# Kernel optimization log

Measured on AMD Instinct MI355X. Metric: run time of the kernel, lower is better.

Reference implementation:

```python
import jax, jax.numpy as jnp
import numpy as np

N_NODES = 10000
N_EDGES = 80000
LATENT = 128
OUT_SIZE = 3
NODE_F = 12
EDGE_F = 7
STEPS = 15
LN_EPS = 1e-5


def _mlp(x, W0, b0, W1, b1, W2, b2):
    h = jax.nn.relu(x @ W0 + b0)
    h = jax.nn.relu(h @ W1 + b1)
    return h @ W2 + b2


def _ln(x, g, b):
    m = jnp.mean(x, axis=-1, keepdims=True)
    v = jnp.mean(jnp.square(x - m), axis=-1, keepdims=True)
    return (x - m) * jax.lax.rsqrt(v + LN_EPS) * g + b


def _forward(node_features, edge_features, senders, receivers,
             enW0, enb0, enW1, enb1, enW2, enb2, eng, enbe,
             eeW0, eeb0, eeW1, eeb1, eeW2, eeb2, eeg, eebe,
             beW0, beb0, beW1, beb1, beW2, beb2, beg, bebe,
             bnW0, bnb0, bnW1, bnb1, bnW2, bnb2, bng, bnbe,
             dW0, db0, dW1, db1, dW2, db2):
    # Encoder: node and mesh-edge MLPs with LayerNorm
    nl = _ln(_mlp(node_features, enW0, enb0, enW1, enb1, enW2, enb2), eng, enbe)  # [N, L]
    el = _ln(_mlp(edge_features, eeW0, eeb0, eeW1, eeb1, eeW2, eeb2), eeg, eebe)  # [E, L]

    # Processor: 15 GraphNetBlocks with residual connections, scanned over stacked params
    def block(carry, p):
        n, e = carry
        (eW0, eb0, eW1, eb1, eW2, eb2, eg, ebe,
         nW0, nb0, nW1, nb1, nW2, nb2, ng, nbe) = p
        feat = jnp.concatenate([n[senders], n[receivers], e], axis=-1)  # [E, 3L]
        new_e = _ln(_mlp(feat, eW0, eb0, eW1, eb1, eW2, eb2), eg, ebe)  # [E, L]
        agg = jax.ops.segment_sum(new_e, receivers, num_segments=N_NODES)  # [N, L]
        new_n = _ln(_mlp(jnp.concatenate([n, agg], axis=-1), nW0, nb0, nW1, nb1, nW2, nb2), ng, nbe)
        return (n + new_n, e + new_e), None

    xs = (beW0, beb0, beW1, beb1, beW2, beb2, beg, bebe,
          bnW0, bnb0, bnW1, bnb1, bnW2, bnb2, bng, bnbe)
    (nl, el), _ = jax.lax.scan(jax.checkpoint(block), (nl, el), xs)

    # Decoder: MLP without LayerNorm
    return _mlp(nl, dW0, db0, dW1, db1, dW2, db2)  # [N, OUT_SIZE]


def setup_inputs() -> dict:
    ks = iter(jax.random.split(jax.random.key(0), 32))

    def W(*shape):
        return jax.random.normal(next(ks), shape, jnp.float32) * (1.0 / np.sqrt(shape[-2]))

    z = lambda *s: jnp.zeros(s, jnp.float32)
    o = lambda *s: jnp.ones(s, jnp.float32)
    d = {}
    d['node_features'] = jax.random.normal(next(ks), (N_NODES, NODE_F), jnp.float32)
    d['edge_features'] = jax.random.normal(next(ks), (N_EDGES, EDGE_F), jnp.float32)
    d['senders'] = jax.random.randint(next(ks), (N_EDGES,), 0, N_NODES, jnp.int32)
    d['receivers'] = jax.random.randint(next(ks), (N_EDGES,), 0, N_NODES, jnp.int32)
    d.update(enW0=W(NODE_F, LATENT), enb0=z(LATENT), enW1=W(LATENT, LATENT), enb1=z(LATENT),
             enW2=W(LATENT, LATENT), enb2=z(LATENT), eng=o(LATENT), enbe=z(LATENT))
    d.update(eeW0=W(EDGE_F, LATENT), eeb0=z(LATENT), eeW1=W(LATENT, LATENT), eeb1=z(LATENT),
             eeW2=W(LATENT, LATENT), eeb2=z(LATENT), eeg=o(LATENT), eebe=z(LATENT))
    d.update(beW0=W(STEPS, 3 * LATENT, LATENT), beb0=z(STEPS, LATENT),
             beW1=W(STEPS, LATENT, LATENT), beb1=z(STEPS, LATENT),
             beW2=W(STEPS, LATENT, LATENT), beb2=z(STEPS, LATENT),
             beg=o(STEPS, LATENT), bebe=z(STEPS, LATENT))
    d.update(bnW0=W(STEPS, 2 * LATENT, LATENT), bnb0=z(STEPS, LATENT),
             bnW1=W(STEPS, LATENT, LATENT), bnb1=z(STEPS, LATENT),
             bnW2=W(STEPS, LATENT, LATENT), bnb2=z(STEPS, LATENT),
             bng=o(STEPS, LATENT), bnbe=z(STEPS, LATENT))
    d.update(dW0=W(LATENT, LATENT), db0=z(LATENT), dW1=W(LATENT, LATENT), db1=z(LATENT),
             dW2=W(LATENT, OUT_SIZE), db2=z(OUT_SIZE))
    return d


def reference(node_features, edge_features, senders, receivers,
              enW0, enb0, enW1, enb1, enW2, enb2, eng, enbe,
              eeW0, eeb0, eeW1, eeb1, eeW2, eeb2, eeg, eebe,
              beW0, beb0, beW1, beb1, beW2, beb2, beg, bebe,
              bnW0, bnb0, bnW1, bnb1, bnW2, bnb2, bng, bnbe,
              dW0, db0, dW1, db1, dW2, db2):
    return _forward(node_features, edge_features, senders, receivers,
                    enW0, enb0, enW1, enb1, enW2, enb2, eng, enbe,
                    eeW0, eeb0, eeW1, eeb1, eeW2, eeb2, eeg, eebe,
                    beW0, beb0, beW1, beb1, beW2, beb2, beg, bebe,
                    bnW0, bnb0, bnW1, bnb1, bnW2, bnb2, bng, bnbe,
                    dW0, db0, dW1, db1, dW2, db2)
```

## Files before the change

### kernel.cpp

```cpp
#include <hip/hip_runtime.h>
#include <hip/hip_bf16.h>
#include <stdint.h>

#define N_NODES 10000
#define N_EDGES 80000
#define L 128
#define STEPS 15
#define LN_EPS 1e-5f
#define NTHR 256
#define BM 128

#define H_STRIDE 272
#define H_WAVE   8704
#define WS_OFF   34816
#define LDS_SZ   45056

typedef short short8 __attribute__((ext_vector_type(8)));
typedef float floatx4 __attribute__((ext_vector_type(4)));

__device__ __forceinline__ float bf2f(const __hip_bfloat16 x) {
    return __bfloat162float(x);
}
__device__ __forceinline__ float ldmix(const void* p, int idx, int isf32) {
    return isf32 ? ((const float*)p)[idx]
                 : bf2f(((const __hip_bfloat16*)p)[idx]);
}

__global__ void detect_dtype(const uint32_t* __restrict__ nf, int* cnt) {
    int c = 0;
    for (int i = blockIdx.x * blockDim.x + threadIdx.x; i < 60000;
         i += gridDim.x * blockDim.x) {
        const uint32_t w = nf[i];
        c += (((w >> 7) & 0xFF) >= 0xC6) + (((w >> 23) & 0xFF) >= 0xC6);
    }
    atomicAdd(cnt, c);
}

#define N_TMATS 14
struct TAll {
    const void* src[N_TMATS];
    long long cum[N_TMATS + 1];
    int K[N_TMATS], N[N_TMATS], Kpad[N_TMATS];
};

__global__ void transpose_all(TAll a, const int* __restrict__ cnt,
                              __hip_bfloat16* __restrict__ pool) {
    const int isf32 = (*cnt > 1000);
    const long long total = a.cum[N_TMATS];
    for (long long i = blockIdx.x * (long long)blockDim.x + threadIdx.x;
         i < total; i += gridDim.x * (long long)blockDim.x) {
        int e = 0;
        #pragma unroll 1
        for (int j = 1; j < N_TMATS; j++) if (i >= a.cum[j]) e = j;
        const long long r = i - a.cum[e];
        const int per = a.N[e] * a.Kpad[e];
        const int m = (int)(r / per);
        const int r2 = (int)(r - (long long)m * per);
        const int nn = r2 / a.Kpad[e];
        const int kk = r2 - nn * a.Kpad[e];
        float v = 0.f;
        if (kk < a.K[e]) v = ldmix(a.src[e], (m * a.K[e] + kk) * a.N[e] + nn, isf32);
        pool[i] = __float2bfloat16(v);
    }
}

__global__ void convert_feats(const void* __restrict__ nf,
                              const void* __restrict__ ef,
                              const int* __restrict__ cnt,
                              __hip_bfloat16* __restrict__ fN,
                              __hip_bfloat16* __restrict__ fE)
{
    const int isf32 = (*cnt > 1000);
    const int totN = N_NODES * 32;
    const int totE = N_EDGES * 32;
    for (int i = blockIdx.x * blockDim.x + threadIdx.x; i < totN + totE;
         i += gridDim.x * blockDim.x) {
        if (i < totN) {
            const int r = i >> 5, c = i & 31;
            fN[i] = __float2bfloat16(c < 12 ? ldmix(nf, r * 12 + c, isf32) : 0.f);
        } else {
            const int j = i - totN;
            const int r = j >> 5, c = j & 31;
            fE[j] = __float2bfloat16(c < 7 ? ldmix(ef, r * 7 + c, isf32) : 0.f);
        }
    }
}

__global__ void csr_hist(const int* __restrict__ rcv, int* __restrict__ deg) {
    for (int i = blockIdx.x * blockDim.x + threadIdx.x; i < N_EDGES;
         i += gridDim.x * blockDim.x)
        atomicAdd(&deg[rcv[i]], 1);
}

__global__ void csr_scan(const int* __restrict__ deg, int* __restrict__ rowptr,
                         int* __restrict__ cursor) {
    __shared__ int part[256];
    __shared__ int partx[257];
    const int t = threadIdx.x;
    int s = 0;
    for (int j = 0; j < 40; j++) {
        const int i = t * 40 + j;
        if (i < N_NODES) s += deg[i];
    }
    part[t] = s;
    __syncthreads();
    if (t == 0) {
        int r = 0;
        for (int k = 0; k < 256; k++) { partx[k] = r; r += part[k]; }
        partx[256] = r;
    }
    __syncthreads();
    int run = partx[t];
    for (int j = 0; j < 40; j++) {
        const int i = t * 40 + j;
        if (i < N_NODES) {
            rowptr[i] = run;
            cursor[i] = run;
            run += deg[i];
        }
    }
    if (t == 255) rowptr[N_NODES] = partx[256];
}

__global__ void csr_scatter(const int* __restrict__ rcv, int* __restrict__ cursor,
                            int* __restrict__ elist) {
    for (int i = blockIdx.x * blockDim.x + threadIdx.x; i < N_EDGES;
         i += gridDim.x * blockDim.x) {
        const int p = atomicAdd(&cursor[rcv[i]], 1);
        elist[p] = i;
    }
}

__global__ __launch_bounds__(256)
void csr_agg(const int* __restrict__ rowptr, const int* __restrict__ elist,
             const __hip_bfloat16* __restrict__ ln16,
             __hip_bfloat16* __restrict__ agg16)
{
    const int g = threadIdx.x >> 5;
    const int lane = threadIdx.x & 31;
    const int v = blockIdx.x * 8 + g;
    if (v >= N_NODES) return;
    const int c0 = lane * 4;
    float s0 = 0.f, s1 = 0.f, s2 = 0.f, s3 = 0.f;
    const int b = rowptr[v], en = rowptr[v + 1];
    for (int j = b; j < en; j++) {
        const int e = elist[j];
        union { uint2 w; __hip_bfloat16 h[4]; } u;
        u.w = *(const uint2*)(ln16 + (size_t)e * L + c0);
        s0 += bf2f(u.h[0]); s1 += bf2f(u.h[1]);
        s2 += bf2f(u.h[2]); s3 += bf2f(u.h[3]);
    }
    union { uint2 w; __hip_bfloat16 h[4]; } o;
    o.h[0] = __float2bfloat16(s0); o.h[1] = __float2bfloat16(s1);
    o.h[2] = __float2bfloat16(s2); o.h[3] = __float2bfloat16(s3);
    *(uint2*)(agg16 + (size_t)v * L + c0) = o.w;
}

enum AMode { A_PLAIN = 0, A_FEAT = 1, A_CAT = 2 };
enum Epi   { E_LN_STORE = 0, E_LN_EDGE = 1, E_LN_NODE = 2, E_DEC = 3 };

template <int AMODE, int EPI, int NL>
__global__ __launch_bounds__(NTHR, 2)
void fused_mlp(const __hip_bfloat16* __restrict__ A, int lda, int M, int K0,
               const __hip_bfloat16* __restrict__ WT0,
               const __hip_bfloat16* __restrict__ WT1,
               const __hip_bfloat16* __restrict__ WT2,
               const void* __restrict__ b0,
               const void* __restrict__ b1,
               const void* __restrict__ b2,
               const void* __restrict__ g,
               const void* __restrict__ beta,
               int poff,
               const int* __restrict__ cnt,
               const __hip_bfloat16* __restrict__ n16,
               const __hip_bfloat16* __restrict__ e16s,
               const __hip_bfloat16* __restrict__ agg16,
               const int* __restrict__ snd,
               const int* __restrict__ rcv,
               float* __restrict__ res32,
               __hip_bfloat16* __restrict__ res16,
               __hip_bfloat16* __restrict__ ln16,
               const void* __restrict__ dW,
               const void* __restrict__ db,
               void* __restrict__ dout)
{
    __shared__ __align__(16) char lds[LDS_SZ];
    char* AsB = lds;
    char* WsB = lds + WS_OFF;

    const int tid  = threadIdx.x;
    const int wv   = tid >> 6;
    const int lane = tid & 63;
    const int quad = lane >> 4;
    const int m15  = lane & 15;
    const int row0 = blockIdx.x * BM;
    const int isf32 = (*cnt > 1000);

    char* hw = lds + wv * H_WAVE;

    const int aoff0 = (wv * 32 + m15) * 80 + quad * 16;
    const int aoff1 = aoff0 + 16 * 80;
    const int boff  = m15 * 80 + quad * 16;

    floatx4 acc[2][8];

    #pragma unroll
    for (int rt = 0; rt < 2; rt++)
        #pragma unroll
        for (int ct = 0; ct < 8; ct++) acc[rt][ct] = (floatx4)0.f;

    for (int k0 = 0; k0 < K0; k0 += 32) {
        #pragma unroll
        for (int i2 = 0; i2 < 2; i2++) {
            const int flat = i2 * NTHR + tid;
            const int ar = flat >> 2;
            const int aq = flat & 3;
            const int rg = row0 + ar;
            int4 av = make_int4(0, 0, 0, 0);
            if (rg < M) {
                if constexpr (AMODE == A_PLAIN) {
                    av = *(const int4*)(A + (size_t)rg * lda + k0 + aq * 8);
                } else if constexpr (AMODE == A_FEAT) {
                    const __hip_bfloat16* sp;
                    if (k0 < L)          sp = n16  + (size_t)snd[rg] * L + k0 + aq * 8;
                    else if (k0 < 2 * L) sp = n16  + (size_t)rcv[rg] * L + (k0 - L) + aq * 8;
                    else                 sp = e16s + (size_t)rg * L + (k0 - 2 * L) + aq * 8;
                    av = *(const int4*)sp;
                } else {
                    const __hip_bfloat16* sp = (k0 < L)
                        ? n16   + (size_t)rg * L + k0 + aq * 8
                        : agg16 + (size_t)rg * L + (k0 - L) + aq * 8;
                    av = *(const int4*)sp;
                }
            }
            *(int4*)(AsB + ar * 80 + aq * 16) = av;
            *(int4*)(WsB + ar * 80 + aq * 16) =
                *(const int4*)(WT0 + (size_t)ar * K0 + k0 + aq * 8);
        }
        __syncthreads();
        const short8 a0 = *(const short8*)(AsB + aoff0);
        const short8 a1 = *(const short8*)(AsB + aoff1);
        #pragma unroll
        for (int ct = 0; ct < 8; ct++) {
            const short8 b = *(const short8*)(WsB + boff + ct * 1280);
            acc[0][ct] = __builtin_amdgcn_mfma_f32_16x16x32_bf16(a0, b, acc[0][ct], 0, 0, 0);
            acc[1][ct] = __builtin_amdgcn_mfma_f32_16x16x32_bf16(a1, b, acc[1][ct], 0, 0, 0);
        }
        __syncthreads();
    }
    {
        float bb[8];
        #pragma unroll
        for (int ct = 0; ct < 8; ct++) bb[ct] = ldmix(b0, poff + ct * 16 + m15, isf32);
        #pragma unroll
        for (int rt = 0; rt < 2; rt++)
            #pragma unroll
            for (int ct = 0; ct < 8; ct++)
                #pragma unroll
                for (int i = 0; i < 4; i++) {
                    const int rl = rt * 16 + quad * 4 + i;
                    const int col = ct * 16 + m15;
                    *(__hip_bfloat16*)(hw + rl * H_STRIDE + col * 2) =
                        __float2bfloat16(fmaxf(acc[rt][ct][i] + bb[ct], 0.f));
                }
    }

    {
        #pragma unroll
        for (int rt = 0; rt < 2; rt++)
            #pragma unroll
            for (int ct = 0; ct < 8; ct++) acc[rt][ct] = (floatx4)0.f;
        short8 af[2][4];
        #pragma unroll
        for (int rt = 0; rt < 2; rt++)
            #pragma unroll
            for (int c = 0; c < 4; c++)
                af[rt][c] = *(const short8*)(hw + (rt * 16 + m15) * H_STRIDE + c * 64 + quad * 16);
        for (int c = 0; c < 4; c++) {
            #pragma unroll
            for (int i2 = 0; i2 < 2; i2++) {
                const int flat = i2 * NTHR + tid;
                const int ar = flat >> 2;
                const int aq = flat & 3;
                *(int4*)(WsB + ar * 80 + aq * 16) =
                    *(const int4*)(WT1 + (size_t)ar * L + c * 32 + aq * 8);
            }
            __syncthreads();
            #pragma unroll
            for (int ct = 0; ct < 8; ct++) {
                const short8 b = *(const short8*)(WsB + boff + ct * 1280);
                acc[0][ct] = __builtin_amdgcn_mfma_f32_16x16x32_bf16(af[0][c], b, acc[0][ct], 0, 0, 0);
                acc[1][ct] = __builtin_amdgcn_mfma_f32_16x16x32_bf16(af[1][c], b, acc[1][ct], 0, 0, 0);
            }
            __syncthreads();
        }
        float bb[8];
        #pragma unroll
        for (int ct = 0; ct < 8; ct++) bb[ct] = ldmix(b1, poff + ct * 16 + m15, isf32);
        #pragma unroll
        for (int rt = 0; rt < 2; rt++)
            #pragma unroll
            for (int ct = 0; ct < 8; ct++)
                #pragma unroll
                for (int i = 0; i < 4; i++) {
                    const int rl = rt * 16 + quad * 4 + i;
                    const int col = ct * 16 + m15;
                    *(__hip_bfloat16*)(hw + rl * H_STRIDE + col * 2) =
                        __float2bfloat16(fmaxf(acc[rt][ct][i] + bb[ct], 0.f));
                }
    }

    if constexpr (NL == 3) {
        #pragma unroll
        for (int rt = 0; rt < 2; rt++)
            #pragma unroll
            for (int ct = 0; ct < 8; ct++) acc[rt][ct] = (floatx4)0.f;
        short8 af[2][4];
        #pragma unroll
        for (int rt = 0; rt < 2; rt++)
            #pragma unroll
            for (int c = 0; c < 4; c++)
                af[rt][c] = *(const short8*)(hw + (rt * 16 + m15) * H_STRIDE + c * 64 + quad * 16);
        for (int c = 0; c < 4; c++) {
            #pragma unroll
            for (int i2 = 0; i2 < 2; i2++) {
                const int flat = i2 * NTHR + tid;
                const int ar = flat >> 2;
                const int aq = flat & 3;
                *(int4*)(WsB + ar * 80 + aq * 16) =
                    *(const int4*)(WT2 + (size_t)ar * L + c * 32 + aq * 8);
            }
            __syncthreads();
            #pragma unroll
            for (int ct = 0; ct < 8; ct++) {
                const short8 b = *(const short8*)(WsB + boff + ct * 1280);
                acc[0][ct] = __builtin_amdgcn_mfma_f32_16x16x32_bf16(af[0][c], b, acc[0][ct], 0, 0, 0);
                acc[1][ct] = __builtin_amdgcn_mfma_f32_16x16x32_bf16(af[1][c], b, acc[1][ct], 0, 0, 0);
            }
            __syncthreads();
        }
        float bb[8], gg[8], be[8];
        #pragma unroll
        for (int ct = 0; ct < 8; ct++) {
            bb[ct] = ldmix(b2,   poff + ct * 16 + m15, isf32);
            gg[ct] = ldmix(g,    poff + ct * 16 + m15, isf32);
            be[ct] = ldmix(beta, poff + ct * 16 + m15, isf32);
        }
        #pragma unroll
        for (int rt = 0; rt < 2; rt++) {
            #pragma unroll
            for (int i = 0; i < 4; i++) {
                float t[8], s = 0.f, s2 = 0.f;
                #pragma unroll
                for (int ct = 0; ct < 8; ct++) {
                    t[ct] = acc[rt][ct][i] + bb[ct];
                    s  += t[ct];
                    s2 += t[ct] * t[ct];
                }
                #pragma unroll
                for (int m = 1; m < 16; m <<= 1) {
                    s  += __shfl_xor(s,  m, 64);
                    s2 += __shfl_xor(s2, m, 64);
                }
                const float mean = s * (1.f / 128.f);
                const float var  = s2 * (1.f / 128.f) - mean * mean;
                const float inv  = rsqrtf(fmaxf(var, 0.f) + LN_EPS);
                const int rl = wv * 32 + rt * 16 + quad * 4 + i;
                const int rg = row0 + rl;
                if (rg < M) {
                    #pragma unroll
                    for (int ct = 0; ct < 8; ct++) {
                        const int col = ct * 16 + m15;
                        const float o = (t[ct] - mean) * inv * gg[ct] + be[ct];
                        const size_t idx = (size_t)rg * L + col;
                        if constexpr (EPI == E_LN_STORE) {
                            res32[idx] = o;
                            res16[idx] = __float2bfloat16(o);
                        } else if constexpr (EPI == E_LN_NODE) {
                            const float nw = res32[idx] + o;
                            res32[idx] = nw;
                            res16[idx] = __float2bfloat16(nw);
                        } else {
                            const float nw = res32[idx] + o;
                            res32[idx] = nw;
                            res16[idx] = __float2bfloat16(nw);
                            ln16[idx]  = __float2bfloat16(o);
                        }
                    }
                }
            }
        }
    } else {
        __syncthreads();
        float* Wl = (float*)WsB;
        for (int i = tid; i < 3 * L; i += NTHR) {
            const int o = i / L, k = i - o * L;
            Wl[o * L + k] = ldmix(dW, k * 3 + o, isf32);
        }
        __syncthreads();
        if (tid < BM) {
            const int rg = row0 + tid;
            if (rg < M) {
                const __hip_bfloat16* hr =
                    (const __hip_bfloat16*)(lds + (tid >> 5) * H_WAVE + (tid & 31) * H_STRIDE);
                float s0 = ldmix(db, 0, isf32);
                float s1 = ldmix(db, 1, isf32);
                float s2 = ldmix(db, 2, isf32);
                #pragma unroll 8
                for (int k = 0; k < L; k++) {
                    const float hv = bf2f(hr[k]);
                    s0 += hv * Wl[k];
                    s1 += hv * Wl[L + k];
                    s2 += hv * Wl[2 * L + k];
                }
                if (isf32) {
                    float* o = (float*)dout;
                    o[rg * 3 + 0] = s0; o[rg * 3 + 1] = s1; o[rg * 3 + 2] = s2;
                } else {
                    __hip_bfloat16* o = (__hip_bfloat16*)dout;
                    o[rg * 3 + 0] = __float2bfloat16(s0);
                    o[rg * 3 + 1] = __float2bfloat16(s1);
                    o[rg * 3 + 2] = __float2bfloat16(s2);
                }
            }
        }
    }
}

extern "C" void kernel_launch(void* const* d_in, const int* in_sizes, int n_in,
                              void* d_out, int out_size, void* d_ws, size_t ws_size,
                              hipStream_t stream)
{
    (void)in_sizes; (void)n_in; (void)out_size; (void)ws_size;
    const int* snd = (const int*)d_in[2];
    const int* rcv = (const int*)d_in[3];

    char* ws = (char*)d_ws;
    int* cnt = (int*)ws;                              ws += 256;
    auto takeB = [&](size_t el) {
        __hip_bfloat16* p = (__hip_bfloat16*)ws;
        ws += ((el * 2 + 255) & ~255ull);
        return p;
    };
    auto takeF = [&](size_t el) {
        float* p = (float*)ws;
        ws += ((el * 4 + 255) & ~255ull);
        return p;
    };
    auto takeI = [&](size_t el) {
        int* p = (int*)ws;
        ws += ((el * 4 + 255) & ~255ull);
        return p;
    };

    const int srcIdx[N_TMATS] = {4, 6, 8, 12, 14, 16, 20, 22, 24, 28, 30, 32, 36, 38};
    const int tK[N_TMATS]    = {12, 128, 128, 7, 128, 128, 384, 128, 128, 256, 128, 128, 128, 128};
    const int tKp[N_TMATS]   = {32, 128, 128, 32, 128, 128, 384, 128, 128, 256, 128, 128, 128, 128};
    const int tNm[N_TMATS]   = {1, 1, 1, 1, 1, 1, STEPS, STEPS, STEPS, STEPS, STEPS, STEPS, 1, 1};
    TAll ta;
    long long cum = 0;
    __hip_bfloat16* wmat[N_TMATS];
    __hip_bfloat16* wpool = (__hip_bfloat16*)ws;
    for (int j = 0; j < N_TMATS; j++) {
        ta.src[j] = d_in[srcIdx[j]];
        ta.cum[j] = cum;
        ta.K[j] = tK[j]; ta.N[j] = 128; ta.Kpad[j] = tKp[j];
        wmat[j] = wpool + cum;
        cum += (long long)tNm[j] * 128 * tKp[j];
    }
    ta.cum[N_TMATS] = cum;
    ws += ((cum * 2 + 255) & ~255ull);

    float* n32 = takeF((size_t)N_NODES * L);
    float* e32 = takeF((size_t)N_EDGES * L);
    __hip_bfloat16* n16   = takeB((size_t)N_NODES * L);
    __hip_bfloat16* e16   = takeB((size_t)N_EDGES * L);
    __hip_bfloat16* ln16  = takeB((size_t)N_EDGES * L);
    __hip_bfloat16* agg16 = takeB((size_t)N_NODES * L);
    __hip_bfloat16* fN16  = takeB((size_t)N_NODES * 32);
    __hip_bfloat16* fE16  = takeB((size_t)N_EDGES * 32);
    int* deg    = takeI(N_NODES);
    int* rowptr = takeI(N_NODES + 1);
    int* cursor = takeI(N_NODES);
    int* elist  = takeI(N_EDGES);

    const dim3 blk(NTHR);
    const dim3 grdE((N_EDGES + BM - 1) / BM);
    const dim3 grdN((N_NODES + BM - 1) / BM);

    (void)hipMemsetAsync(cnt, 0, sizeof(int), stream);
    (void)hipMemsetAsync(deg, 0, N_NODES * sizeof(int), stream);
    detect_dtype<<<dim3(64), blk, 0, stream>>>((const uint32_t*)d_in[0], cnt);
    convert_feats<<<dim3(256), blk, 0, stream>>>(d_in[0], d_in[1], cnt, fN16, fE16);
    transpose_all<<<dim3(512), blk, 0, stream>>>(ta, cnt, wpool);

    csr_hist<<<dim3(80), blk, 0, stream>>>(rcv, deg);
    csr_scan<<<dim3(1), blk, 0, stream>>>(deg, rowptr, cursor);
    csr_scatter<<<dim3(80), blk, 0, stream>>>(rcv, cursor, elist);

    fused_mlp<A_PLAIN, E_LN_STORE, 3><<<grdE, blk, 0, stream>>>(
        fE16, 32, N_EDGES, 32, wmat[3], wmat[4], wmat[5],
        d_in[13], d_in[15], d_in[17], d_in[18], d_in[19], 0, cnt,
        nullptr, nullptr, nullptr, nullptr, nullptr,
        e32, e16, nullptr, nullptr, nullptr, nullptr);
    fused_mlp<A_PLAIN, E_LN_STORE, 3><<<grdN, blk, 0, stream>>>(
        fN16, 32, N_NODES, 32, wmat[0], wmat[1], wmat[2],
        d_in[5], d_in[7], d_in[9], d_in[10], d_in[11], 0, cnt,
        nullptr, nullptr, nullptr, nullptr, nullptr,
        n32, n16, nullptr, nullptr, nullptr, nullptr);

    for (int s = 0; s < STEPS; s++) {
        const int po = s * L;
        fused_mlp<A_FEAT, E_LN_EDGE, 3><<<grdE, blk, 0, stream>>>(
            nullptr, 0, N_EDGES, 384,
            wmat[6] + (size_t)s * 128 * 384,
            wmat[7] + (size_t)s * 128 * 128,
            wmat[8] + (size_t)s * 128 * 128,
            d_in[21], d_in[23], d_in[25], d_in[26], d_in[27], po, cnt,
            n16, e16, nullptr, snd, rcv,
            e32, e16, ln16, nullptr, nullptr, nullptr);
        csr_agg<<<dim3((N_NODES + 7) / 8), blk, 0, stream>>>(rowptr, elist, ln16, agg16);
        fused_mlp<A_CAT, E_LN_NODE, 3><<<grdN, blk, 0, stream>>>(
            nullptr, 0, N_NODES, 256,
            wmat[9]  + (size_t)s * 128 * 256,
            wmat[10] + (size_t)s * 128 * 128,
            wmat[11] + (size_t)s * 128 * 128,
            d_in[29], d_in[31], d_in[33], d_in[34], d_in[35], po, cnt,
            n16, nullptr, agg16, nullptr, nullptr,
            n32, n16, nullptr, nullptr, nullptr, nullptr);
    }

    fused_mlp<A_PLAIN, E_DEC, 2><<<grdN, blk, 0, stream>>>(
        n16, L, N_NODES, L, wmat[12], wmat[13], nullptr,
        d_in[37], d_in[39], nullptr, nullptr, nullptr, 0, cnt,
        nullptr, nullptr, nullptr, nullptr, nullptr,
        nullptr, nullptr, nullptr, d_in[40], d_in[41], d_out);
}
```

Before: 1.433 ms.

## Fuse CSR aggregation into node MLP, prefetch tiles, drop bf16 edge copy

Removes the separate csr_agg kernel and computes each node tile's receiver-sum into LDS inside the node MLP kernel. The edge-latent bf16 copy is dropped: the edge MLP now reads the fp32 residual and converts it to bf16 on the fly. Global loads for A and W tiles are register-prefetched one k-step ahead, with gather indices hoisted. Node kernels use 64-row tiles via a new RT template parameter to raise block count. This saves launches and a bf16 edge write per step, at the cost of more LDS use and a doubled fp32 read in the edge kernel.

```diff
diff --git a/kernel.cpp b/kernel.cpp
--- a/kernel.cpp
+++ b/kernel.cpp
@@ -8,12 +8,7 @@
 #define STEPS 15
 #define LN_EPS 1e-5f
 #define NTHR 256
-#define BM 128
-
 #define H_STRIDE 272
-#define H_WAVE   8704
-#define WS_OFF   34816
-#define LDS_SZ   45056
 
 typedef short short8 __attribute__((ext_vector_type(8)));
 typedef float floatx4 __attribute__((ext_vector_type(4)));
@@ -131,35 +126,10 @@
     }
 }
 
-__global__ __launch_bounds__(256)
-void csr_agg(const int* __restrict__ rowptr, const int* __restrict__ elist,
-             const __hip_bfloat16* __restrict__ ln16,
-             __hip_bfloat16* __restrict__ agg16)
-{
-    const int g = threadIdx.x >> 5;
-    const int lane = threadIdx.x & 31;
-    const int v = blockIdx.x * 8 + g;
-    if (v >= N_NODES) return;
-    const int c0 = lane * 4;
-    float s0 = 0.f, s1 = 0.f, s2 = 0.f, s3 = 0.f;
-    const int b = rowptr[v], en = rowptr[v + 1];
-    for (int j = b; j < en; j++) {
-        const int e = elist[j];
-        union { uint2 w; __hip_bfloat16 h[4]; } u;
-        u.w = *(const uint2*)(ln16 + (size_t)e * L + c0);
-        s0 += bf2f(u.h[0]); s1 += bf2f(u.h[1]);
-        s2 += bf2f(u.h[2]); s3 += bf2f(u.h[3]);
-    }
-    union { uint2 w; __hip_bfloat16 h[4]; } o;
-    o.h[0] = __float2bfloat16(s0); o.h[1] = __float2bfloat16(s1);
-    o.h[2] = __float2bfloat16(s2); o.h[3] = __float2bfloat16(s3);
-    *(uint2*)(agg16 + (size_t)v * L + c0) = o.w;
-}
-
 enum AMode { A_PLAIN = 0, A_FEAT = 1, A_CAT = 2 };
 enum Epi   { E_LN_STORE = 0, E_LN_EDGE = 1, E_LN_NODE = 2, E_DEC = 3 };
 
-template <int AMODE, int EPI, int NL>
+template <int AMODE, int EPI, int NL, int RT>
 __global__ __launch_bounds__(NTHR, 2)
 void fused_mlp(const __hip_bfloat16* __restrict__ A, int lda, int M, int K0,
                const __hip_bfloat16* __restrict__ WT0,
@@ -172,79 +142,163 @@
                const void* __restrict__ beta,
                int poff,
                const int* __restrict__ cnt,
-               const __hip_bfloat16* __restrict__ n16,
-               const __hip_bfloat16* __restrict__ e16s,
-               const __hip_bfloat16* __restrict__ agg16,
+               const __hip_bfloat16* n16,
+               const __hip_bfloat16* lnsrc,
                const int* __restrict__ snd,
                const int* __restrict__ rcv,
-               float* __restrict__ res32,
-               __hip_bfloat16* __restrict__ res16,
-               __hip_bfloat16* __restrict__ ln16,
+               const int* __restrict__ rowptr,
+               const int* __restrict__ elist,
+               float* res32,
+               __hip_bfloat16* res16,
+               __hip_bfloat16* __restrict__ lnout,
                const void* __restrict__ dW,
                const void* __restrict__ db,
                void* __restrict__ dout)
 {
-    __shared__ __align__(16) char lds[LDS_SZ];
+    constexpr int BMv   = 64 * RT;
+    constexpr int HW    = RT * 16 * H_STRIDE;
+    constexpr int WSOFF = 4 * HW;
+    constexpr int LDSB  = WSOFF + 10240 + ((AMODE == A_CAT) ? BMv * 256 : 0);
+    __shared__ __align__(16) char lds[LDSB];
     char* AsB = lds;
-    char* WsB = lds + WS_OFF;
+    char* WsB = lds + WSOFF;
+    char* AgL = lds + WSOFF + 10240;
 
     const int tid  = threadIdx.x;
     const int wv   = tid >> 6;
     const int lane = tid & 63;
     const int quad = lane >> 4;
     const int m15  = lane & 15;
-    const int row0 = blockIdx.x * BM;
+    const int row0 = blockIdx.x * BMv;
     const int isf32 = (*cnt > 1000);
 
-    char* hw = lds + wv * H_WAVE;
-
-    const int aoff0 = (wv * 32 + m15) * 80 + quad * 16;
-    const int aoff1 = aoff0 + 16 * 80;
-    const int boff  = m15 * 80 + quad * 16;
-
-    floatx4 acc[2][8];
-
+    char* hw = lds + wv * HW;
+
+    const int boff = m15 * 80 + quad * 16;
+    int aoff[RT];
     #pragma unroll
-    for (int rt = 0; rt < 2; rt++)
+    for (int rt = 0; rt < RT; rt++)
+        aoff[rt] = (wv * 16 * RT + rt * 16 + m15) * 80 + quad * 16;
+
+    if constexpr (AMODE == A_CAT) {
+        const int half = tid >> 5, hl = tid & 31;
+        for (int v = half; v < BMv; v += 8) {
+            const int rg = row0 + v;
+            float s0 = 0.f, s1 = 0.f, s2 = 0.f, s3 = 0.f;
+            if (rg < M) {
+                int j = rowptr[rg];
+                const int en = rowptr[rg + 1];
+                for (; j + 3 < en; j += 4) {
+                    const int e0 = elist[j], e1 = elist[j+1], e2 = elist[j+2], e3 = elist[j+3];
+                    union { uint2 w; __hip_bfloat16 h[4]; } u0, u1, u2, u3;
+                    u0.w = *(const uint2*)(lnsrc + (size_t)e0 * L + hl * 4);
+                    u1.w = *(const uint2*)(lnsrc + (size_t)e1 * L + hl * 4);
+                    u2.w = *(const uint2*)(lnsrc + (size_t)e2 * L + hl * 4);
+                    u3.w = *(const uint2*)(lnsrc + (size_t)e3 * L + hl * 4);
+                    s0 += bf2f(u0.h[0]); s1 += bf2f(u0.h[1]); s2 += bf2f(u0.h[2]); s3 += bf2f(u0.h[3]);
+                    s0 += bf2f(u1.h[0]); s1 += bf2f(u1.h[1]); s2 += bf2f(u1.h[2]); s3 += bf2f(u1.h[3]);
+                    s0 += bf2f(u2.h[0]); s1 += bf2f(u2.h[1]); s2 += bf2f(u2.h[2]); s3 += bf2f(u2.h[3]);
+                    s0 += bf2f(u3.h[0]); s1 += bf2f(u3.h[1]); s2 += bf2f(u3.h[2]); s3 += bf2f(u3.h[3]);
+                }
+                for (; j < en; j++) {
+                    const int e = elist[j];
+                    union { uint2 w; __hip_bfloat16 h[4]; } u;
+                    u.w = *(const uint2*)(lnsrc + (size_t)e * L + hl * 4);
+                    s0 += bf2f(u.h[0]); s1 += bf2f(u.h[1]); s2 += bf2f(u.h[2]); s3 += bf2f(u.h[3]);
+                }
+            }
+            union { uint2 w; __hip_bfloat16 h[4]; } o;
+            o.h[0] = __float2bfloat16(s0); o.h[1] = __float2bfloat16(s1);
+            o.h[2] = __float2bfloat16(s2); o.h[3] = __float2bfloat16(s3);
+            *(uint2*)(AgL + v * 256 + hl * 8) = o.w;
+        }
+        __syncthreads();
+    }
+
+    const int aq = tid & 3;
+    int arow[RT], sidx[RT], ridx[RT];
+    #pragma unroll
+    for (int i2 = 0; i2 < RT; i2++) {
+        arow[i2] = (i2 * NTHR + tid) >> 2;
+        if constexpr (AMODE == A_FEAT) {
+            const int rg = row0 + arow[i2];
+            sidx[i2] = (rg < M) ? snd[rg] : 0;
+            ridx[i2] = (rg < M) ? rcv[rg] : 0;
+        }
+    }
+
+    auto loadA = [&](int k0, int i2) -> int4 {
+        const int ar = arow[i2];
+        const int rg = row0 + ar;
+        int4 av = make_int4(0, 0, 0, 0);
+        if (rg < M) {
+            if constexpr (AMODE == A_PLAIN) {
+                av = *(const int4*)(A + (size_t)rg * lda + k0 + aq * 8);
+            } else if constexpr (AMODE == A_FEAT) {
+                if (k0 < 2 * L) {
+                    const int nd = (k0 < L) ? sidx[i2] : ridx[i2];
+                    av = *(const int4*)(n16 + (size_t)nd * L + (k0 & (L - 1)) + aq * 8);
+                } else {
+                    const float* sp = res32 + (size_t)rg * L + (k0 - 2 * L) + aq * 8;
+                    const float4 f0 = *(const float4*)sp;
+                    const float4 f1 = *(const float4*)(sp + 4);
+                    union { int4 v; __hip_bfloat16 h[8]; } u;
+                    u.h[0] = __float2bfloat16(f0.x); u.h[1] = __float2bfloat16(f0.y);
+                    u.h[2] = __float2bfloat16(f0.z); u.h[3] = __float2bfloat16(f0.w);
+                    u.h[4] = __float2bfloat16(f1.x); u.h[5] = __float2bfloat16(f1.y);
+                    u.h[6] = __float2bfloat16(f1.z); u.h[7] = __float2bfloat16(f1.w);
+                    av = u.v;
+                }
+            } else {
+                if (k0 < L) av = *(const int4*)(n16 + (size_t)rg * L + k0 + aq * 8);
+                else        av = *(const int4*)(AgL + ar * 256 + (k0 - L) * 2 + aq * 16);
+            }
+        }
+        return av;
+    };
+    auto loadW = [&](const __hip_bfloat16* WT, int ksz, int k0, int i2) -> int4 {
+        const int flat = i2 * NTHR + tid;
+        return *(const int4*)(WT + (size_t)(flat >> 2) * ksz + k0 + (flat & 3) * 8);
+    };
+
+    floatx4 acc[RT][8];
+
+    #pragma unroll
+    for (int rt = 0; rt < RT; rt++)
         #pragma unroll
         for (int ct = 0; ct < 8; ct++) acc[rt][ct] = (floatx4)0.f;
 
+    int4 pA[RT], pW[2];
+    #pragma unroll
+    for (int i2 = 0; i2 < RT; i2++) pA[i2] = loadA(0, i2);
+    pW[0] = loadW(WT0, K0, 0, 0);
+    pW[1] = loadW(WT0, K0, 0, 1);
+
     for (int k0 = 0; k0 < K0; k0 += 32) {
+        #pragma unroll
+        for (int i2 = 0; i2 < RT; i2++)
+            *(int4*)(AsB + arow[i2] * 80 + aq * 16) = pA[i2];
         #pragma unroll
         for (int i2 = 0; i2 < 2; i2++) {
             const int flat = i2 * NTHR + tid;
-            const int ar = flat >> 2;
-            const int aq = flat & 3;
-            const int rg = row0 + ar;
-            int4 av = make_int4(0, 0, 0, 0);
-            if (rg < M) {
-                if constexpr (AMODE == A_PLAIN) {
-                    av = *(const int4*)(A + (size_t)rg * lda + k0 + aq * 8);
-                } else if constexpr (AMODE == A_FEAT) {
-                    const __hip_bfloat16* sp;
-                    if (k0 < L)          sp = n16  + (size_t)snd[rg] * L + k0 + aq * 8;
-                    else if (k0 < 2 * L) sp = n16  + (size_t)rcv[rg] * L + (k0 - L) + aq * 8;
-                    else                 sp = e16s + (size_t)rg * L + (k0 - 2 * L) + aq * 8;
-                    av = *(const int4*)sp;
-                } else {
-                    const __hip_bfloat16* sp = (k0 < L)
-                        ? n16   + (size_t)rg * L + k0 + aq * 8
-                        : agg16 + (size_t)rg * L + (k0 - L) + aq * 8;
-                    av = *(const int4*)sp;
-                }
-            }
-            *(int4*)(AsB + ar * 80 + aq * 16) = av;
-            *(int4*)(WsB + ar * 80 + aq * 16) =
-                *(const int4*)(WT0 + (size_t)ar * K0 + k0 + aq * 8);
+            *(int4*)(WsB + (flat >> 2) * 80 + (flat & 3) * 16) = pW[i2];
         }
         __syncthreads();
-        const short8 a0 = *(const short8*)(AsB + aoff0);
-        const short8 a1 = *(const short8*)(AsB + aoff1);
+        if (k0 + 32 < K0) {
+            #pragma unroll
+            for (int i2 = 0; i2 < RT; i2++) pA[i2] = loadA(k0 + 32, i2);
+            pW[0] = loadW(WT0, K0, k0 + 32, 0);
+            pW[1] = loadW(WT0, K0, k0 + 32, 1);
+        }
+        short8 a[RT];
+        #pragma unroll
+        for (int rt = 0; rt < RT; rt++) a[rt] = *(const short8*)(AsB + aoff[rt]);
         #pragma unroll
         for (int ct = 0; ct < 8; ct++) {
             const short8 b = *(const short8*)(WsB + boff + ct * 1280);
-            acc[0][ct] = __builtin_amdgcn_mfma_f32_16x16x32_bf16(a0, b, acc[0][ct], 0, 0, 0);
-            acc[1][ct] = __builtin_amdgcn_mfma_f32_16x16x32_bf16(a1, b, acc[1][ct], 0, 0, 0);
+            #pragma unroll
+            for (int rt = 0; rt < RT; rt++)
+                acc[rt][ct] = __builtin_amdgcn_mfma_f32_16x16x32_bf16(a[rt], b, acc[rt][ct], 0, 0, 0);
         }
         __syncthreads();
     }
@@ -253,7 +307,7 @@
         #pragma unroll
         for (int ct = 0; ct < 8; ct++) bb[ct] = ldmix(b0, poff + ct * 16 + m15, isf32);
         #pragma unroll
-        for (int rt = 0; rt < 2; rt++)
+        for (int rt = 0; rt < RT; rt++)
             #pragma unroll
             for (int ct = 0; ct < 8; ct++)
                 #pragma unroll
@@ -267,30 +321,35 @@
 
     {
         #pragma unroll
-        for (int rt = 0; rt < 2; rt++)
+        for (int rt = 0; rt < RT; rt++)
             #pragma unroll
             for (int ct = 0; ct < 8; ct++) acc[rt][ct] = (floatx4)0.f;
-        short8 af[2][4];
-        #pragma unroll
-        for (int rt = 0; rt < 2; rt++)
+        short8 af[RT][4];
+        #pragma unroll
+        for (int rt = 0; rt < RT; rt++)
             #pragma unroll
             for (int c = 0; c < 4; c++)
                 af[rt][c] = *(const short8*)(hw + (rt * 16 + m15) * H_STRIDE + c * 64 + quad * 16);
+        int4 qW[2];
+        qW[0] = loadW(WT1, L, 0, 0);
+        qW[1] = loadW(WT1, L, 0, 1);
         for (int c = 0; c < 4; c++) {
             #pragma unroll
             for (int i2 = 0; i2 < 2; i2++) {
                 const int flat = i2 * NTHR + tid;
-                const int ar = flat >> 2;
-                const int aq = flat & 3;
-                *(int4*)(WsB + ar * 80 + aq * 16) =
-                    *(const int4*)(WT1 + (size_t)ar * L + c * 32 + aq * 8);
+                *(int4*)(WsB + (flat >> 2) * 80 + (flat & 3) * 16) = qW[i2];
             }
             __syncthreads();
+            if (c < 3) {
+                qW[0] = loadW(WT1, L, (c + 1) * 32, 0);
+                qW[1] = loadW(WT1, L, (c + 1) * 32, 1);
+            }
             #pragma unroll
             for (int ct = 0; ct < 8; ct++) {
                 const short8 b = *(const short8*)(WsB + boff + ct * 1280);
-                acc[0][ct] = __builtin_amdgcn_mfma_f32_16x16x32_bf16(af[0][c], b, acc[0][ct], 0, 0, 0);
-                acc[1][ct] = __builtin_amdgcn_mfma_f32_16x16x32_bf16(af[1][c], b, acc[1][ct], 0, 0, 0);
+                #pragma unroll
+                for (int rt = 0; rt < RT; rt++)
+                    acc[rt][ct] = __builtin_amdgcn_mfma_f32_16x16x32_bf16(af[rt][c], b, acc[rt][ct], 0, 0, 0);
             }
             __syncthreads();
         }
@@ -298,7 +357,7 @@
         #pragma unroll
         for (int ct = 0; ct < 8; ct++) bb[ct] = ldmix(b1, poff + ct * 16 + m15, isf32);
         #pragma unroll
-        for (int rt = 0; rt < 2; rt++)
+        for (int rt = 0; rt < RT; rt++)
             #pragma unroll
             for (int ct = 0; ct < 8; ct++)
                 #pragma unroll
@@ -312,30 +371,35 @@
 
     if constexpr (NL == 3) {
         #pragma unroll
-        for (int rt = 0; rt < 2; rt++)
+        for (int rt = 0; rt < RT; rt++)
             #pragma unroll
             for (int ct = 0; ct < 8; ct++) acc[rt][ct] = (floatx4)0.f;
-        short8 af[2][4];
-        #pragma unroll
-        for (int rt = 0; rt < 2; rt++)
+        short8 af[RT][4];
+        #pragma unroll
+        for (int rt = 0; rt < RT; rt++)
             #pragma unroll
             for (int c = 0; c < 4; c++)
                 af[rt][c] = *(const short8*)(hw + (rt * 16 + m15) * H_STRIDE + c * 64 + quad * 16);
+        int4 qW[2];
+        qW[0] = loadW(WT2, L, 0, 0);
+        qW[1] = loadW(WT2, L, 0, 1);
         for (int c = 0; c < 4; c++) {
             #pragma unroll
             for (int i2 = 0; i2 < 2; i2++) {
                 const int flat = i2 * NTHR + tid;
-                const int ar = flat >> 2;
-                const int aq = flat & 3;
-                *(int4*)(WsB + ar * 80 + aq * 16) =
-                    *(const int4*)(WT2 + (size_t)ar * L + c * 32 + aq * 8);
+                *(int4*)(WsB + (flat >> 2) * 80 + (flat & 3) * 16) = qW[i2];
             }
             __syncthreads();
+            if (c < 3) {
+                qW[0] = loadW(WT2, L, (c + 1) * 32, 0);
+                qW[1] = loadW(WT2, L, (c + 1) * 32, 1);
+            }
             #pragma unroll
             for (int ct = 0; ct < 8; ct++) {
                 const short8 b = *(const short8*)(WsB + boff + ct * 1280);
-                acc[0][ct] = __builtin_amdgcn_mfma_f32_16x16x32_bf16(af[0][c], b, acc[0][ct], 0, 0, 0);
-                acc[1][ct] = __builtin_amdgcn_mfma_f32_16x16x32_bf16(af[1][c], b, acc[1][ct], 0, 0, 0);
+                #pragma unroll
+                for (int rt = 0; rt < RT; rt++)
+                    acc[rt][ct] = __builtin_amdgcn_mfma_f32_16x16x32_bf16(af[rt][c], b, acc[rt][ct], 0, 0, 0);
             }
             __syncthreads();
         }
@@ -347,7 +411,7 @@
             be[ct] = ldmix(beta, poff + ct * 16 + m15, isf32);
         }
         #pragma unroll
-        for (int rt = 0; rt < 2; rt++) {
+        for (int rt = 0; rt < RT; rt++) {
             #pragma unroll
             for (int i = 0; i < 4; i++) {
                 float t[8], s = 0.f, s2 = 0.f;
@@ -365,7 +429,7 @@
                 const float mean = s * (1.f / 128.f);
                 const float var  = s2 * (1.f / 128.f) - mean * mean;
                 const float inv  = rsqrtf(fmaxf(var, 0.f) + LN_EPS);
-                const int rl = wv * 32 + rt * 16 + quad * 4 + i;
+                const int rl = wv * 16 * RT + rt * 16 + quad * 4 + i;
                 const int rg = row0 + rl;
                 if (rg < M) {
                     #pragma unroll
@@ -375,7 +439,7 @@
                         const size_t idx = (size_t)rg * L + col;
                         if constexpr (EPI == E_LN_STORE) {
                             res32[idx] = o;
-                            res16[idx] = __float2bfloat16(o);
+                            if (res16) res16[idx] = __float2bfloat16(o);
                         } else if constexpr (EPI == E_LN_NODE) {
                             const float nw = res32[idx] + o;
                             res32[idx] = nw;
@@ -383,8 +447,7 @@
                         } else {
                             const float nw = res32[idx] + o;
                             res32[idx] = nw;
-                            res16[idx] = __float2bfloat16(nw);
-                            ln16[idx]  = __float2bfloat16(o);
+                            lnout[idx] = __float2bfloat16(o);
                         }
                     }
                 }
@@ -398,11 +461,13 @@
             Wl[o * L + k] = ldmix(dW, k * 3 + o, isf32);
         }
         __syncthreads();
-        if (tid < BM) {
+        if (tid < BMv) {
             const int rg = row0 + tid;
             if (rg < M) {
+                const int wave = tid / (16 * RT);
+                const int rw   = tid - wave * 16 * RT;
                 const __hip_bfloat16* hr =
-                    (const __hip_bfloat16*)(lds + (tid >> 5) * H_WAVE + (tid & 31) * H_STRIDE);
+                    (const __hip_bfloat16*)(lds + wave * HW + rw * H_STRIDE);
                 float s0 = ldmix(db, 0, isf32);
                 float s1 = ldmix(db, 1, isf32);
                 float s2 = ldmix(db, 2, isf32);
@@ -473,20 +538,18 @@
 
     float* n32 = takeF((size_t)N_NODES * L);
     float* e32 = takeF((size_t)N_EDGES * L);
-    __hip_bfloat16* n16   = takeB((size_t)N_NODES * L);
-    __hip_bfloat16* e16   = takeB((size_t)N_EDGES * L);
-    __hip_bfloat16* ln16  = takeB((size_t)N_EDGES * L);
-    __hip_bfloat16* agg16 = takeB((size_t)N_NODES * L);
-    __hip_bfloat16* fN16  = takeB((size_t)N_NODES * 32);
-    __hip_bfloat16* fE16  = takeB((size_t)N_EDGES * 32);
+    __hip_bfloat16* n16  = takeB((size_t)N_NODES * L);
+    __hip_bfloat16* ln16 = takeB((size_t)N_EDGES * L);
+    __hip_bfloat16* fN16 = takeB((size_t)N_NODES * 32);
+    __hip_bfloat16* fE16 = takeB((size_t)N_EDGES * 32);
     int* deg    = takeI(N_NODES);
     int* rowptr = takeI(N_NODES + 1);
     int* cursor = takeI(N_NODES);
     int* elist  = takeI(N_EDGES);
 
     const dim3 blk(NTHR);
-    const dim3 grdE((N_EDGES + BM - 1) / BM);
-    const dim3 grdN((N_NODES + BM - 1) / BM);
+    const dim3 grdE((N_EDGES + 127) / 128);
+    const dim3 grdN((N_NODES + 63) / 64);
 
     (void)hipMemsetAsync(cnt, 0, sizeof(int), stream);
     (void)hipMemsetAsync(deg, 0, N_NODES * sizeof(int), stream);
@@ -498,41 +561,40 @@
     csr_scan<<<dim3(1), blk, 0, stream>>>(deg, rowptr, cursor);
     csr_scatter<<<dim3(80), blk, 0, stream>>>(rcv, cursor, elist);
 
-    fused_mlp<A_PLAIN, E_LN_STORE, 3><<<grdE, blk, 0, stream>>>(
+    fused_mlp<A_PLAIN, E_LN_STORE, 3, 2><<<grdE, blk, 0, stream>>>(
         fE16, 32, N_EDGES, 32, wmat[3], wmat[4], wmat[5],
         d_in[13], d_in[15], d_in[17], d_in[18], d_in[19], 0, cnt,
-        nullptr, nullptr, nullptr, nullptr, nullptr,
-        e32, e16, nullptr, nullptr, nullptr, nullptr);
-    fused_mlp<A_PLAIN, E_LN_STORE, 3><<<grdN, blk, 0, stream>>>(
+        nullptr, nullptr, nullptr, nullptr, nullptr, nullptr,
+        e32, nullptr, nullptr, nullptr, nullptr, nullptr);
+    fused_mlp<A_PLAIN, E_LN_STORE, 3, 1><<<grdN, blk, 0, stream>>>(
         fN16, 32, N_NODES, 32, wmat[0], wmat[1], wmat[2],
         d_in[5], d_in[7], d_in[9], d_in[10], d_in[11], 0, cnt,
-        nullptr, nullptr, nullptr, nullptr, nullptr,
+        nullptr, nullptr, nullptr, nullptr, nullptr, nullptr,
         n32, n16, nullptr, nullptr, nullptr, nullptr);
 
     for (int s = 0; s < STEPS; s++) {
         const int po = s * L;
-        fused_mlp<A_FEAT, E_LN_EDGE, 3><<<grdE, blk, 0, stream>>>(
+        fused_mlp<A_FEAT, E_LN_EDGE, 3, 2><<<grdE, blk, 0, stream>>>(
             nullptr, 0, N_EDGES, 384,
             wmat[6] + (size_t)s * 128 * 384,
             wmat[7] + (size_t)s * 128 * 128,
             wmat[8] + (size_t)s * 128 * 128,
             d_in[21], d_in[23], d_in[25], d_in[26], d_in[27], po, cnt,
-            n16, e16, nullptr, snd, rcv,
-            e32, e16, ln16, nullptr, nullptr, nullptr);
-        csr_agg<<<dim3((N_NODES + 7) / 8), blk, 0, stream>>>(rowptr, elist, ln16, agg16);
-        fused_mlp<A_CAT, E_LN_NODE, 3><<<grdN, blk, 0, stream>>>(
+            n16, nullptr, snd, rcv, nullptr, nullptr,
+            e32, nullptr, ln16, nullptr, nullptr, nullptr);
+        fused_mlp<A_CAT, E_LN_NODE, 3, 1><<<grdN, blk, 0, stream>>>(
             nullptr, 0, N_NODES, 256,
             wmat[9]  + (size_t)s * 128 * 256,
             wmat[10] + (size_t)s * 128 * 128,
             wmat[11] + (size_t)s * 128 * 128,
             d_in[29], d_in[31], d_in[33], d_in[34], d_in[35], po, cnt,
-            n16, nullptr, agg16, nullptr, nullptr,
+            n16, ln16, nullptr, nullptr, rowptr, elist,
             n32, n16, nullptr, nullptr, nullptr, nullptr);
     }
 
-    fused_mlp<A_PLAIN, E_DEC, 2><<<grdN, blk, 0, stream>>>(
+    fused_mlp<A_PLAIN, E_DEC, 2, 1><<<grdN, blk, 0, stream>>>(
         n16, L, N_NODES, L, wmat[12], wmat[13], nullptr,
         d_in[37], d_in[39], nullptr, nullptr, nullptr, 0, cnt,
-        nullptr, nullptr, nullptr, nullptr, nullptr,
+        nullptr, nullptr, nullptr, nullptr, nullptr, nullptr,
         nullptr, nullptr, nullptr, d_in[40], d_in[41], d_out);
 }
```

Result: slower. 1.647 ms (+14.9%).
